# Kernel tuning notes

Hardware: AMD Instinct MI355X
Metric: run time of the kernel (lower is better)

The kernel has to match this reference:

```python
import jax, jax.numpy as jnp
import numpy as np

P, D, Q = 2, 1, 2  # ARIMA(p, d, q) orders from init_kwargs
B_SZ, T_SEQ = 8192, 4096


def setup_inputs() -> dict:
    key = jax.random.key(0)
    k1, k2, k3, k4 = jax.random.split(key, 4)
    y = jax.random.normal(k1, (B_SZ, T_SEQ), dtype=jnp.float32)
    # small coefficients keep the MA recurrence numerically stable
    phi = jax.random.normal(k2, (P,), dtype=jnp.float32) * 0.1
    theta = jax.random.normal(k3, (Q,), dtype=jnp.float32) * 0.1
    mu = jax.random.normal(k4, (1,), dtype=jnp.float32) * 0.1
    return {"y": y, "phi": phi, "theta": theta, "mu": mu}


def reference(y, phi, theta, mu):
    B, Tseq = y.shape
    T = Tseq - D
    yd = y[:, D:] - y[:, :-D]  # d-th difference, (B, T)
    # AR term depends only on y -> precompute for all t in [P, T):
    #   ar[:, t-P] = sum_i phi[i] * y[:, D + t - 1 - i]   (flip + dot)
    ar = jnp.zeros((B, T - P), y.dtype)
    for i in range(P):  # P is tiny and static
        ar = ar + phi[i] * y[:, D + P - 1 - i: D + T - 1 - i]
    target = yd[:, P:] - mu[0] - ar  # (B, T-P): eps_t = target_t - theta . eps_window

    def step(win, tgt):
        eps_t = tgt - win @ theta  # (B,)
        win = jnp.concatenate([eps_t[:, None], win[:, :-1]], axis=1)
        return win, eps_t

    win0 = jnp.zeros((B, Q), y.dtype)  # eps buffer starts at zero
    _, eps_seq = jax.lax.scan(step, win0, target.T)  # (T-P, B)
    eps = eps_seq.T  # (B, T-P)
    # torch code returns eps[:, p:] of the (B, T+q) buffer -> trailing Q zeros
    return jnp.concatenate([eps, jnp.zeros((B, Q), y.dtype)], axis=1)
```

## Files before the change

kernel.cpp:

```cpp
#include <hip/hip_runtime.h>


#define TSEQ   4096
#define TOUT   4095
#define NJ     4093
#define CHUNK  256
#define NCHUNK 16
#define TILE   64
#define PITCH  65
#define WARM   61

#define LGKM_FENCE() do { \
    asm volatile("s_waitcnt lgkmcnt(0)" ::: "memory"); \
    __builtin_amdgcn_sched_barrier(0); \
} while (0)

__global__ __launch_bounds__(64) void arima_eps_sw(
    const float* __restrict__ y,
    const float* __restrict__ phi,
    const float* __restrict__ theta,
    const float* __restrict__ mu,
    float* __restrict__ out)
{
    __shared__ float lds[TILE][PITCH];

    const int lane = threadIdx.x;
    const int g = blockIdx.x >> 4;
    const int c = blockIdx.x & (NCHUNK - 1);
    const int rowbase = g * 64;

    const float p0 = phi[0], p1v = phi[1];
    const float q0 = theta[0], q1 = theta[1];
    const float m  = mu[0];
    const float c1 = 1.0f + p0;
    const float A  = q0 * q0 - q1;
    const float Bc = q0 * q1;

    const float* __restrict__ Y = y + (size_t)rowbase * TSEQ;
    float* __restrict__ O       = out + (size_t)rowbase * TOUT;

    const int j0 = c * CHUNK;
    const int j1 = min(j0 + CHUNK, NJ);
    const int jw = max(j0 - WARM, 0);

    const int srow = lane >> 4;
    const int scol = (lane & 15) << 2;

    float4 stg[16];
    int sdcol;

    auto stage = [&](int tbase) {
        int off = tbase + scol;
        if (off > TSEQ - 4) off = TSEQ - 4;
        sdcol = off - tbase;
        #pragma unroll
        for (int qq = 0; qq < 16; ++qq) {
            const int r = qq * 4 + srow;
            stg[qq] = *reinterpret_cast<const float4*>(&Y[(size_t)r * TSEQ + off]);
        }
    };
    auto lds_write = [&]() {
        #pragma unroll
        for (int qq = 0; qq < 16; ++qq) {
            const int r = qq * 4 + srow;
            lds[sdcol + 0][r] = stg[qq].x;
            lds[sdcol + 1][r] = stg[qq].y;
            lds[sdcol + 2][r] = stg[qq].z;
            lds[sdcol + 3][r] = stg[qq].w;
        }
    };

    float yp1, yp2;
    float e1 = 0.f, e2 = 0.f, e3 = 0.f;
    float tp = 0.f;

    auto step8 = [&](int cb) {
        float yv[8];
        #pragma unroll
        for (int k = 0; k < 8; ++k) yv[k] = lds[cb + k][lane];
        float tg[8];
        {
            float pa = yp2, pb = yp1;
            #pragma unroll
            for (int k = 0; k < 8; ++k) {
                float t = __builtin_fmaf(-c1, pb, yv[k]);
                t = __builtin_fmaf(-p1v, pa, t);
                tg[k] = t - m;
                pa = pb; pb = yv[k];
            }
        }
        yp2 = yv[6]; yp1 = yv[7];
        float T[8];
        T[0] = __builtin_fmaf(-q0, tp, tg[0]);
        #pragma unroll
        for (int k = 1; k < 8; ++k) T[k] = __builtin_fmaf(-q0, tg[k - 1], tg[k]);
        tp = tg[7];
        float ev[8];
        ev[0] = __builtin_fmaf(A, e2,    __builtin_fmaf(Bc, e3,    T[0]));
        ev[1] = __builtin_fmaf(A, e1,    __builtin_fmaf(Bc, e2,    T[1]));
        ev[2] = __builtin_fmaf(A, ev[0], __builtin_fmaf(Bc, e1,    T[2]));
        ev[3] = __builtin_fmaf(A, ev[1], __builtin_fmaf(Bc, ev[0], T[3]));
        ev[4] = __builtin_fmaf(A, ev[2], __builtin_fmaf(Bc, ev[1], T[4]));
        ev[5] = __builtin_fmaf(A, ev[3], __builtin_fmaf(Bc, ev[2], T[5]));
        ev[6] = __builtin_fmaf(A, ev[4], __builtin_fmaf(Bc, ev[3], T[6]));
        ev[7] = __builtin_fmaf(A, ev[5], __builtin_fmaf(Bc, ev[4], T[7]));
        e3 = ev[5]; e2 = ev[6]; e1 = ev[7];
        #pragma unroll
        for (int k = 0; k < 8; ++k) lds[cb + k][lane] = ev[k];
    };

    auto dump = [&](int jt, int jcur, int tb) {
        const int jd  = max(jt, j0);
        const int je  = min(jcur, j1);
        const int cnt = je - jd;
        if (cnt <= 0) return;
        const int dcol = jd + 3 - tb;
        const bool on  = lane < cnt;
        float* op = O + jd + lane;
        #pragma unroll 8
        for (int r = 0; r < 64; ++r) {
            if (on) op[(size_t)r * TOUT] = lds[dcol + lane][r];
        }
    };

    int tb = jw;
    stage(tb);
    lds_write();
    LGKM_FENCE();
    {
        float yv0[8];
        #pragma unroll
        for (int k = 0; k < 8; ++k) yv0[k] = lds[k][lane];
        yp2 = yv0[1]; yp1 = yv0[2];
        float ev[5];
        #pragma unroll
        for (int k = 3; k < 8; ++k) {
            float t = __builtin_fmaf(-c1, yp1, yv0[k]);
            t = __builtin_fmaf(-p1v, yp2, t);
            t -= m;
            float e = __builtin_fmaf(-q0, e1, t);
            e = __builtin_fmaf(-q1, e2, e);
            ev[k - 3] = e;
            e3 = e2; e2 = e1; e1 = e;
            tp = t;
            yp2 = yp1; yp1 = yv0[k];
        }
        #pragma unroll
        for (int k = 3; k < 8; ++k) lds[k][lane] = ev[k - 3];
    }
    step8(8); step8(16); step8(24); step8(32); step8(40); step8(48); step8(56);
    int jt = jw;
    int j  = jw + 61;

    for (;;) {
        const bool more = (j < j1);
        if (more) stage(tb + TILE);
        LGKM_FENCE();
        dump(jt, j, tb);
        if (!more) break;
        LGKM_FENCE();
        lds_write();
        LGKM_FENCE();
        tb += TILE;
        jt = tb - 3;
        step8(0); step8(8); step8(16); step8(24);
        step8(32); step8(40); step8(48); step8(56);
        j = jt + TILE;
    }

    if (c == NCHUNK - 1) {
        O[(size_t)lane * TOUT + NJ]     = 0.f;
        O[(size_t)lane * TOUT + NJ + 1] = 0.f;
    }
}

extern "C" void kernel_launch(void* const* d_in, const int* in_sizes, int n_in,
                              void* d_out, int out_size, void* d_ws, size_t ws_size,
                              hipStream_t stream) {
    const float* y     = (const float*)d_in[0];
    const float* phi   = (const float*)d_in[1];
    const float* theta = (const float*)d_in[2];
    const float* mu    = (const float*)d_in[3];
    float* out         = (float*)d_out;

    int B = in_sizes[0] / TSEQ;
    int rowgroups = B / 64;
    dim3 block(64);
    dim3 grid(rowgroups * NCHUNK);
    arima_eps_sw<<<grid, block, 0, stream>>>(y, phi, theta, mu, out);
}
```

Measured before the change: 68.17 us.

## Double-buffer LDS tiles with two-ahead register prefetch and half-size tiles

Halves the time tile from 64 to 32 columns and splits LDS into two buffers. Global loads for tile t+3 go into alternating register sets while the current tile is computed and dumped. The goal is to hide global-load latency behind the serial recurrence and the output stores, instead of stalling on each stage-then-write cycle. In exchange it doubles staging registers, adds more loop iterations with their fences, and changes the store pattern to 32 columns by 2 row halves.

```diff
diff --git a/kernel.cpp b/kernel.cpp
--- a/kernel.cpp
+++ b/kernel.cpp
@@ -6,7 +6,7 @@
 #define NJ     4093
 #define CHUNK  256
 #define NCHUNK 16
-#define TILE   64
+#define TILE   32
 #define PITCH  65
 #define WARM   61
 
@@ -15,14 +15,36 @@
     __builtin_amdgcn_sched_barrier(0); \
 } while (0)
 
-__global__ __launch_bounds__(64) void arima_eps_sw(
+#define STAGE(SET, SD, TBASE) do { \
+    int off_ = (TBASE) + scol; \
+    if (off_ > TSEQ - 4) off_ = TSEQ - 4;    \
+    SD = off_ - (TBASE);                     \
+    _Pragma("unroll") \
+    for (int qq = 0; qq < 8; ++qq) { \
+        const int r_ = qq * 8 + srow; \
+        SET[qq] = *reinterpret_cast<const float4*>(&Y[(size_t)r_ * TSEQ + off_]); \
+    } \
+} while (0)
+
+#define LDSW(SET, SD, BI) do { \
+    _Pragma("unroll") \
+    for (int qq = 0; qq < 8; ++qq) { \
+        const int r_ = qq * 8 + srow; \
+        lds[BI][SD + 0][r_] = SET[qq].x; \
+        lds[BI][SD + 1][r_] = SET[qq].y; \
+        lds[BI][SD + 2][r_] = SET[qq].z; \
+        lds[BI][SD + 3][r_] = SET[qq].w; \
+    } \
+} while (0)
+
+__global__ __launch_bounds__(64) void arima_eps_db(
     const float* __restrict__ y,
     const float* __restrict__ phi,
     const float* __restrict__ theta,
     const float* __restrict__ mu,
     float* __restrict__ out)
 {
-    __shared__ float lds[TILE][PITCH];
+    __shared__ float lds[2][TILE][PITCH];
 
     const int lane = threadIdx.x;
     const int g = blockIdx.x >> 4;
@@ -42,42 +64,22 @@
     const int j0 = c * CHUNK;
     const int j1 = min(j0 + CHUNK, NJ);
     const int jw = max(j0 - WARM, 0);
-
-    const int srow = lane >> 4;
-    const int scol = (lane & 15) << 2;
-
-    float4 stg[16];
-    int sdcol;
-
-    auto stage = [&](int tbase) {
-        int off = tbase + scol;
-        if (off > TSEQ - 4) off = TSEQ - 4;
-        sdcol = off - tbase;
-        #pragma unroll
-        for (int qq = 0; qq < 16; ++qq) {
-            const int r = qq * 4 + srow;
-            stg[qq] = *reinterpret_cast<const float4*>(&Y[(size_t)r * TSEQ + off]);
-        }
-    };
-    auto lds_write = [&]() {
-        #pragma unroll
-        for (int qq = 0; qq < 16; ++qq) {
-            const int r = qq * 4 + srow;
-            lds[sdcol + 0][r] = stg[qq].x;
-            lds[sdcol + 1][r] = stg[qq].y;
-            lds[sdcol + 2][r] = stg[qq].z;
-            lds[sdcol + 3][r] = stg[qq].w;
-        }
-    };
+    const int NT = (j1 + 3 - jw + TILE - 1) / TILE;
+
+    const int srow = lane >> 3;
+    const int scol = (lane & 7) << 2;
+
+    float4 s0[8], s1[8];
+    int sd0, sd1;
 
     float yp1, yp2;
     float e1 = 0.f, e2 = 0.f, e3 = 0.f;
     float tp = 0.f;
 
-    auto step8 = [&](int cb) {
+    auto step8 = [&](float (*Bf)[PITCH], int cb) {
         float yv[8];
         #pragma unroll
-        for (int k = 0; k < 8; ++k) yv[k] = lds[cb + k][lane];
+        for (int k = 0; k < 8; ++k) yv[k] = Bf[cb + k][lane];
         float tg[8];
         {
             float pa = yp2, pb = yp1;
@@ -106,31 +108,35 @@
         ev[7] = __builtin_fmaf(A, ev[5], __builtin_fmaf(Bc, ev[4], T[7]));
         e3 = ev[5]; e2 = ev[6]; e1 = ev[7];
         #pragma unroll
-        for (int k = 0; k < 8; ++k) lds[cb + k][lane] = ev[k];
+        for (int k = 0; k < 8; ++k) Bf[cb + k][lane] = ev[k];
     };
 
-    auto dump = [&](int jt, int jcur, int tb) {
+    auto dump = [&](float (*Bf)[PITCH], int jt, int jcur, int tb) {
         const int jd  = max(jt, j0);
         const int je  = min(jcur, j1);
         const int cnt = je - jd;
         if (cnt <= 0) return;
         const int dcol = jd + 3 - tb;
-        const bool on  = lane < cnt;
-        float* op = O + jd + lane;
-        #pragma unroll 8
-        for (int r = 0; r < 64; ++r) {
-            if (on) op[(size_t)r * TOUT] = lds[dcol + lane][r];
+        const int col  = lane & 31;
+        const int rh   = lane >> 5;
+        const bool on  = col < cnt;
+        #pragma unroll
+        for (int r2 = 0; r2 < 32; ++r2) {
+            const int r = r2 * 2 + rh;
+            if (on) O[(size_t)r * TOUT + jd + col] = Bf[dcol + col][r];
         }
     };
 
     int tb = jw;
-    stage(tb);
-    lds_write();
+    STAGE(s0, sd0, tb);
+    LDSW(s0, sd0, 0);
+    if (NT > 1) STAGE(s1, sd1, tb + TILE);
+    if (NT > 2) STAGE(s0, sd0, tb + 2 * TILE);
     LGKM_FENCE();
     {
         float yv0[8];
         #pragma unroll
-        for (int k = 0; k < 8; ++k) yv0[k] = lds[k][lane];
+        for (int k = 0; k < 8; ++k) yv0[k] = lds[0][k][lane];
         yp2 = yv0[1]; yp1 = yv0[2];
         float ev[5];
         #pragma unroll
@@ -146,27 +152,33 @@
             yp2 = yp1; yp1 = yv0[k];
         }
         #pragma unroll
-        for (int k = 3; k < 8; ++k) lds[k][lane] = ev[k - 3];
+        for (int k = 3; k < 8; ++k) lds[0][k][lane] = ev[k - 3];
+        step8(lds[0], 8); step8(lds[0], 16); step8(lds[0], 24);
     }
-    step8(8); step8(16); step8(24); step8(32); step8(40); step8(48); step8(56);
+    LGKM_FENCE();
     int jt = jw;
-    int j  = jw + 61;
-
-    for (;;) {
-        const bool more = (j < j1);
-        if (more) stage(tb + TILE);
-        LGKM_FENCE();
-        dump(jt, j, tb);
-        if (!more) break;
-        LGKM_FENCE();
-        lds_write();
+    int j  = jw + TILE - 3;
+
+    for (int t = 0; t + 1 < NT; ++t) {
+        dump(lds[t & 1], jt, j, tb);
+        if (((t + 1) & 1) == 0) {
+            LDSW(s0, sd0, 0);
+            if (t + 3 < NT) STAGE(s0, sd0, tb + 3 * TILE);
+        } else {
+            LDSW(s1, sd1, 1);
+            if (t + 3 < NT) STAGE(s1, sd1, tb + 3 * TILE);
+        }
         LGKM_FENCE();
         tb += TILE;
         jt = tb - 3;
-        step8(0); step8(8); step8(16); step8(24);
-        step8(32); step8(40); step8(48); step8(56);
+        {
+            float (*Bf)[PITCH] = lds[(t + 1) & 1];
+            step8(Bf, 0); step8(Bf, 8); step8(Bf, 16); step8(Bf, 24);
+        }
         j = jt + TILE;
+        LGKM_FENCE();
     }
+    dump(lds[(NT - 1) & 1], jt, j, tb);
 
     if (c == NCHUNK - 1) {
         O[(size_t)lane * TOUT + NJ]     = 0.f;
@@ -187,5 +199,5 @@
     int rowgroups = B / 64;
     dim3 block(64);
     dim3 grid(rowgroups * NCHUNK);
-    arima_eps_sw<<<grid, block, 0, stream>>>(y, phi, theta, mu, out);
+    arima_eps_db<<<grid, block, 0, stream>>>(y, phi, theta, mu, out);
 }
```

After: 83.44 us. 22.4% more time.

## Drop register-staged prefetch and restructure dump into half-wave row pairs

Applied to the files above, without the earlier changes.

Removes the register staging that prefetched the next tile's global loads while the previous tile was written out, and instead loads each tile straight into LDS after the dump finishes, using __syncthreads in place of manual lgkmcnt fences. The dump now has each half-wave write 32 columns for alternating rows, with a second pass when more than 32 columns are valid, rather than 64 lanes striding over all rows. This frees the 16 float4 staging registers and simplifies synchronisation, but gives up overlap between global loads and output stores, so load latency lands directly on the serial path.

```diff
diff --git a/kernel.cpp b/kernel.cpp
--- a/kernel.cpp
+++ b/kernel.cpp
@@ -10,12 +10,7 @@
 #define PITCH  65
 #define WARM   61
 
-#define LGKM_FENCE() do { \
-    asm volatile("s_waitcnt lgkmcnt(0)" ::: "memory"); \
-    __builtin_amdgcn_sched_barrier(0); \
-} while (0)
-
-__global__ __launch_bounds__(64) void arima_eps_sw(
+__global__ __launch_bounds__(64) void arima_eps_r7(
     const float* __restrict__ y,
     const float* __restrict__ phi,
     const float* __restrict__ theta,
@@ -46,27 +41,19 @@
     const int srow = lane >> 4;
     const int scol = (lane & 15) << 2;
 
-    float4 stg[16];
-    int sdcol;
-
-    auto stage = [&](int tbase) {
+    auto load_tile = [&](int tbase) {
         int off = tbase + scol;
         if (off > TSEQ - 4) off = TSEQ - 4;
-        sdcol = off - tbase;
+        const int sd = off - tbase;
         #pragma unroll
         for (int qq = 0; qq < 16; ++qq) {
             const int r = qq * 4 + srow;
-            stg[qq] = *reinterpret_cast<const float4*>(&Y[(size_t)r * TSEQ + off]);
-        }
-    };
-    auto lds_write = [&]() {
-        #pragma unroll
-        for (int qq = 0; qq < 16; ++qq) {
-            const int r = qq * 4 + srow;
-            lds[sdcol + 0][r] = stg[qq].x;
-            lds[sdcol + 1][r] = stg[qq].y;
-            lds[sdcol + 2][r] = stg[qq].z;
-            lds[sdcol + 3][r] = stg[qq].w;
+            const float4 v = *reinterpret_cast<const float4*>(
+                &Y[(size_t)r * TSEQ + off]);
+            lds[sd + 0][r] = v.x;
+            lds[sd + 1][r] = v.y;
+            lds[sd + 2][r] = v.z;
+            lds[sd + 3][r] = v.w;
         }
     };
 
@@ -115,18 +102,28 @@
         const int cnt = je - jd;
         if (cnt <= 0) return;
         const int dcol = jd + 3 - tb;
-        const bool on  = lane < cnt;
-        float* op = O + jd + lane;
-        #pragma unroll 8
-        for (int r = 0; r < 64; ++r) {
-            if (on) op[(size_t)r * TOUT] = lds[dcol + lane][r];
+        const int col  = lane & 31;
+        const int rh   = lane >> 5;
+        const bool on  = col < cnt;
+        #pragma unroll
+        for (int r2 = 0; r2 < 32; ++r2) {
+            const int r = r2 * 2 + rh;
+            if (on) O[(size_t)r * TOUT + jd + col] = lds[dcol + col][r];
+        }
+        if (cnt > 32) {
+            const int col2 = col + 32;
+            const bool on2 = col2 < cnt;
+            #pragma unroll
+            for (int r2 = 0; r2 < 32; ++r2) {
+                const int r = r2 * 2 + rh;
+                if (on2) O[(size_t)r * TOUT + jd + col2] = lds[dcol + col2][r];
+            }
         }
     };
 
     int tb = jw;
-    stage(tb);
-    lds_write();
-    LGKM_FENCE();
+    load_tile(tb);
+    __syncthreads();
     {
         float yv0[8];
         #pragma unroll
@@ -150,22 +147,21 @@
     }
     step8(8); step8(16); step8(24); step8(32); step8(40); step8(48); step8(56);
     int jt = jw;
-    int j  = jw + 61;
+    int j  = jw + TILE - 3;
+    __syncthreads();
+    dump(jt, j, tb);
 
-    for (;;) {
-        const bool more = (j < j1);
-        if (more) stage(tb + TILE);
-        LGKM_FENCE();
-        dump(jt, j, tb);
-        if (!more) break;
-        LGKM_FENCE();
-        lds_write();
-        LGKM_FENCE();
+    while (j < j1) {
+        __syncthreads();
         tb += TILE;
+        load_tile(tb);
+        __syncthreads();
         jt = tb - 3;
         step8(0); step8(8); step8(16); step8(24);
         step8(32); step8(40); step8(48); step8(56);
         j = jt + TILE;
+        __syncthreads();
+        dump(jt, j, tb);
     }
 
     if (c == NCHUNK - 1) {
@@ -187,5 +183,5 @@
     int rowgroups = B / 64;
     dim3 block(64);
     dim3 grid(rowgroups * NCHUNK);
-    arima_eps_sw<<<grid, block, 0, stream>>>(y, phi, theta, mu, out);
+    arima_eps_r7<<<grid, block, 0, stream>>>(y, phi, theta, mu, out);
 }
```

Measured after the change: 71.78 us. 1.05x slower.
